# Performance work log

Hardware: AMD Instinct MI355X
Metric: run time of the kernel (lower is better)

The kernel has to match this reference:

```python
import jax, jax.numpy as jnp
import numpy as np
import math

B, S, D, H, L = 256, 256, 256, 4, 2
DH = D // H
NITEMS = 50000
EPS = 1e-5


def setup_inputs() -> dict:
    key = jax.random.key(0)
    ks = jax.random.split(key, 16)
    w = lambda k, shape, scale: (jax.random.normal(k, shape, jnp.float32) * scale)
    return {
        "input_ids": jax.random.randint(ks[0], (B, S), 0, NITEMS),
        "item_emb": w(ks[1], (NITEMS, D), 0.02),
        "pos_emb": w(ks[2], (S, D), 0.02),
        "Wq": w(ks[3], (L, D, D), 0.05),
        "bq": jnp.zeros((L, D), jnp.float32),
        "Wk": w(ks[4], (L, D, D), 0.05),
        "bk": jnp.zeros((L, D), jnp.float32),
        "Wv": w(ks[5], (L, D, D), 0.05),
        "bv": jnp.zeros((L, D), jnp.float32),
        "Wo": w(ks[6], (L, D, D), 0.05),
        "bo": jnp.zeros((L, D), jnp.float32),
        "W1": w(ks[7], (L, D, 4 * D), 0.05),
        "b1": jnp.zeros((L, 4 * D), jnp.float32),
        "W2": w(ks[8], (L, 4 * D, D), 0.05),
        "b2": jnp.zeros((L, D), jnp.float32),
    }


def _layer_norm(x):
    mu = jnp.mean(x, axis=-1, keepdims=True)
    var = jnp.mean(jnp.square(x - mu), axis=-1, keepdims=True)
    return (x - mu) * jax.lax.rsqrt(var + EPS)


def reference(input_ids, item_emb, pos_emb, Wq, bq, Wk, bk, Wv, bv,
              Wo, bo, W1, b1, W2, b2):
    Bn, Sn = input_ids.shape
    dtype = item_emb.dtype
    # attention bias: padding (id>0) AND causal; (1-mask)*-10000
    pad = (input_ids > 0).astype(dtype)                       # [B,S]
    causal = jnp.tril(jnp.ones((Sn, Sn), dtype))              # [S,S]
    mask = pad[:, None, None, :] * causal[None, None]         # [B,1,S,S]
    attn_bias = (1.0 - mask) * -10000.0

    # input embedding (dropout is identity in eval)
    x = _layer_norm(item_emb[input_ids] + pos_emb[None])      # [B,S,D]
    total = x
    scale = 1.0 / math.sqrt(DH)

    for l in range(L):
        # --- self-attention ---
        def heads(z):  # [B,S,D] -> [B,H,S,DH]
            return z.reshape(Bn, Sn, H, DH).transpose(0, 2, 1, 3)
        q = heads(x @ Wq[l] + bq[l])
        k = heads(x @ Wk[l] + bk[l])
        v = heads(x @ Wv[l] + bv[l])
        scores = jnp.einsum('bhqd,bhkd->bhqk', q, k) * scale + attn_bias
        probs = jax.nn.softmax(scores, axis=-1)
        ctx = jnp.einsum('bhqk,bhkd->bhqd', probs, v)
        ctx = ctx.transpose(0, 2, 1, 3).reshape(Bn, Sn, D)
        h = _layer_norm(ctx @ Wo[l] + bo[l] + x)
        # --- FFN (no residual in IntermediateLayer) ---
        ffn = jax.nn.gelu(h @ W1[l] + b1[l], approximate=False) @ W2[l] + b2[l]
        x = _layer_norm(ffn)
        total = total + x

    return total
```

## Files before the change

kernel.cpp:

```cpp
#include <hip/hip_runtime.h>
#include <math.h>

typedef __attribute__((ext_vector_type(8))) short short8;
typedef __attribute__((ext_vector_type(4))) short shortx4;
typedef __attribute__((ext_vector_type(4))) int   intx4;
typedef __attribute__((ext_vector_type(4))) float floatx4;

#define BQ 256
#define SQ 256
#define DQ 256
#define HQ 4
#define DHQ 64

__device__ __forceinline__ short f2bf(float f) {
  union { float f; unsigned u; } c; c.f = f;
  unsigned r = c.u + 0x7fffu + ((c.u >> 16) & 1u);
  return (short)(r >> 16);
}
__device__ __forceinline__ float bf2f(short s) {
  union { unsigned u; float f; } c; c.u = ((unsigned)(unsigned short)s) << 16;
  return c.f;
}
__device__ __forceinline__ float gelu_fast(float x) {
  float t = x * (0.7978845608f + 0.0356774081f * x * x);
  return x / (1.0f + __expf(-2.0f * t));
}

__device__ __forceinline__ void async16(const void* g, void* l) {
  __builtin_amdgcn_global_load_lds(
      (const __attribute__((address_space(1))) void*)g,
      (__attribute__((address_space(3))) void*)l, 16, 0, 0);
}

__global__ __launch_bounds__(256) void wconv_kernel(const float* __restrict__ W,
    short* __restrict__ Wt, int K, int N, int total) {
  int idx = blockIdx.x * 256 + threadIdx.x;
  if (idx >= total) return;
  int nk = N * K;
  int l = idx / nk;
  int r = idx - l * nk;
  int n = r / K;
  int k = r - n * K;
  Wt[idx] = f2bf(W[(size_t)l * nk + (size_t)k * N + n]);
}

__global__ __launch_bounds__(256) void wconv_qkv_kernel(const float* __restrict__ Wq,
    const float* __restrict__ Wk, const float* __restrict__ Wv, short* __restrict__ Wt) {
  int idx = blockIdx.x * 256 + threadIdx.x;
  int l = idx / 196608;
  int r = idx - l * 196608;
  int which = r / 65536;
  int e = r & 65535;
  int n = e >> 8, k = e & 255;
  const float* W = (which == 0) ? Wq : ((which == 1) ? Wk : Wv);
  Wt[idx] = f2bf(W[l * 65536 + k * 256 + n]);
}

__global__ __launch_bounds__(256) void bconv_kernel(const float* __restrict__ bq,
    const float* __restrict__ bk, const float* __restrict__ bv, float* __restrict__ dst) {
  int i = blockIdx.x * 256 + threadIdx.x;
  int l = i / 768, r = i - l * 768;
  const float* src = (r < 256) ? bq : ((r < 512) ? bk : bv);
  dst[i] = src[l * 256 + (r & 255)];
}

__global__ __launch_bounds__(256) void embed_kernel(const int* __restrict__ ids,
    const float* __restrict__ item, const float* __restrict__ pos,
    short* __restrict__ xb, float* __restrict__ tot) {
  const int tid = threadIdx.x, lane = tid & 63, w = tid >> 6;
  const int row = blockIdx.x * 4 + w;
  const int s = row & (SQ - 1);
  const int id = ids[row];
  floatx4 a = *(const floatx4*)(item + (size_t)id * DQ + lane * 4);
  floatx4 p = *(const floatx4*)(pos + (size_t)s * DQ + lane * 4);
  float v[4];
#pragma unroll
  for (int i = 0; i < 4; ++i) v[i] = a[i] + p[i];
  float sm = v[0] + v[1] + v[2] + v[3];
  float ss = v[0]*v[0] + v[1]*v[1] + v[2]*v[2] + v[3]*v[3];
#pragma unroll
  for (int off = 32; off; off >>= 1) { sm += __shfl_xor(sm, off); ss += __shfl_xor(ss, off); }
  float mu = sm * (1.0f / DQ);
  float var = ss * (1.0f / DQ) - mu * mu;
  float rs = rsqrtf(var + 1e-5f);
  shortx4 o; floatx4 y;
#pragma unroll
  for (int i = 0; i < 4; ++i) { y[i] = (v[i] - mu) * rs; o[i] = f2bf(y[i]); }
  *(shortx4*)(xb + (size_t)row * DQ + lane * 4) = o;
  *(floatx4*)(tot + (size_t)row * DQ + lane * 4) = y;
}

__global__ __launch_bounds__(512, 4) void gemm_kernel(
    const short* __restrict__ A, const short* __restrict__ Bt,
    const float* __restrict__ bias, const short* __restrict__ res,
    short* __restrict__ out, float* __restrict__ tot, short* __restrict__ vt,
    int M, int N, int K, int act, int ln, int chunked) {
  __shared__ short smem[12288];
  short* As = smem;
  short* Bs = smem + 4096;
  float* redS  = (float*)(smem + 8448);
  float* redS2 = redS + 512;
  const int tid = threadIdx.x, lane = tid & 63, w = tid >> 6;
  const int lane15 = lane & 15, quad = lane >> 4;
  const int wm = w & 1, wn = w >> 1;
  const int bm = blockIdx.y, bn = blockIdx.x;

  const int rA = lane >> 2;
  const int swzA = (rA & 3) ^ ((rA >> 2) & 3);
  const int gA = ((lane & 3) ^ swzA) * 8;
  const short* Ag  = A  + (size_t)(bm * 128 + w * 16 + rA) * K + gA;
  const short* Bg0 = Bt + (size_t)(bn * 256 + w * 32 + rA) * K + gA;
  const short* Bg1 = Bg0 + (size_t)16 * K;

  const int qs = ((quad ^ ((lane15 & 3) ^ ((lane15 >> 2) & 3))) * 8);

  floatx4 acc[4][4] = {};
  const int nk = K >> 5;
  for (int kb = 0; kb < nk; ++kb) {
    const int k0 = kb * 32;
    async16(Ag + k0, &As[w * 512]);
    async16(Bg0 + k0, &Bs[w * 1024]);
    async16(Bg1 + k0, &Bs[w * 1024 + 512]);
    __syncthreads();
    short8 af[4], bfr[4];
#pragma unroll
    for (int i = 0; i < 4; ++i) {
      af[i]  = *(const short8*)&As[(wm * 64 + i * 16 + lane15) * 32 + qs];
      bfr[i] = *(const short8*)&Bs[(wn * 64 + i * 16 + lane15) * 32 + qs];
    }
#pragma unroll
    for (int i = 0; i < 4; ++i)
#pragma unroll
      for (int j = 0; j < 4; ++j)
        acc[i][j] = __builtin_amdgcn_mfma_f32_16x16x32_bf16(bfr[j], af[i], acc[i][j], 0, 0, 0);
    __syncthreads();
  }

  float sum_[4], sq_[4];
#pragma unroll
  for (int i = 0; i < 4; ++i) { sum_[i] = 0.0f; sq_[i] = 0.0f; }
#pragma unroll
  for (int i = 0; i < 4; ++i) {
    size_t rowg = (size_t)bm * 128 + wm * 64 + i * 16 + lane15;
#pragma unroll
    for (int j = 0; j < 4; ++j) {
      int nloc = wn * 64 + j * 16 + quad * 4;
      floatx4 b4 = *(const floatx4*)(bias + bn * 256 + nloc);
      shortx4 r4;
      if (res) r4 = *(const shortx4*)(res + rowg * 256 + nloc);
#pragma unroll
      for (int r = 0; r < 4; ++r) {
        float z = acc[i][j][r] + b4[r];
        if (res) z += bf2f(r4[r]);
        if (act) z = gelu_fast(z);
        acc[i][j][r] = z;
        if (ln) { sum_[i] += z; sq_[i] += z * z; }
      }
    }
  }

  if (ln) {
#pragma unroll
    for (int i = 0; i < 4; ++i) {
      sum_[i] += __shfl_xor(sum_[i], 16); sum_[i] += __shfl_xor(sum_[i], 32);
      sq_[i]  += __shfl_xor(sq_[i], 16);  sq_[i]  += __shfl_xor(sq_[i], 32);
    }
    if (quad == 0) {
#pragma unroll
      for (int i = 0; i < 4; ++i) {
        int lr = wm * 64 + i * 16 + lane15;
        redS[lr * 4 + wn] = sum_[i];
        redS2[lr * 4 + wn] = sq_[i];
      }
    }
    __syncthreads();
#pragma unroll
    for (int i = 0; i < 4; ++i) {
      int lr = wm * 64 + i * 16 + lane15;
      float s = redS[lr * 4] + redS[lr * 4 + 1] + redS[lr * 4 + 2] + redS[lr * 4 + 3];
      float q = redS2[lr * 4] + redS2[lr * 4 + 1] + redS2[lr * 4 + 2] + redS2[lr * 4 + 3];
      float mu = s * (1.0f / 256.0f);
      float var = q * (1.0f / 256.0f) - mu * mu;
      float rs = rsqrtf(var + 1e-5f);
      size_t rowg = (size_t)bm * 128 + wm * 64 + i * 16 + lane15;
#pragma unroll
      for (int j = 0; j < 4; ++j) {
        int nloc = wn * 64 + j * 16 + quad * 4;
        floatx4 y;
#pragma unroll
        for (int r = 0; r < 4; ++r) y[r] = (acc[i][j][r] - mu) * rs;
        acc[i][j] = y;
        if (tot) {
          floatx4* tp = (floatx4*)(tot + rowg * 256 + nloc);
          floatx4 t = *tp;
#pragma unroll
          for (int r = 0; r < 4; ++r) t[r] += y[r];
          *tp = t;
        }
      }
    }
  }

  const int vtrans = (vt != nullptr) && (bn == 2);

#pragma unroll
  for (int i = 0; i < 4; ++i) {
    __syncthreads();
    int lr = wm * 16 + lane15;
#pragma unroll
    for (int j = 0; j < 4; ++j) {
      shortx4 o;
#pragma unroll
      for (int r = 0; r < 4; ++r) o[r] = f2bf(acc[i][j][r]);
      *(shortx4*)&smem[lr * 264 + wn * 64 + j * 16 + quad * 4] = o;
    }
    __syncthreads();
    if (vtrans) {
      int d = tid & 255;
      int grp = tid >> 8;
      short vv[16];
#pragma unroll
      for (int rr = 0; rr < 16; ++rr) vv[rr] = smem[(grp * 16 + rr) * 264 + d];
      size_t row = ((size_t)((bm >> 1) * 256 + d)) * 256 + (bm & 1) * 128 + grp * 64 + i * 16;
      *(short8*)(vt + row) = *(short8*)&vv[0];
      *(short8*)(vt + row + 8) = *(short8*)&vv[8];
    } else {
#pragma unroll
      for (int it = 0; it < 2; ++it) {
        int t2 = tid + it * 512;
        int lr2 = t2 >> 5, c = (t2 & 31) * 8;
        short8 v = *(const short8*)&smem[lr2 * 264 + c];
        size_t rowg = (size_t)bm * 128 + (lr2 >> 4) * 64 + i * 16 + (lr2 & 15);
        short* dst = chunked ? out + (size_t)bn * M * 256 + rowg * 256 + c
                             : out + rowg * (size_t)N + bn * 256 + c;
        *(short8*)dst = v;
      }
    }
  }
}

__global__ __launch_bounds__(256, 4) void attn_kernel(
    const short* __restrict__ qg, const short* __restrict__ kg,
    const short* __restrict__ vtg, const int* __restrict__ ids,
    short* __restrict__ ctxg) {
  __shared__ short lds[20480];
  const int tid = threadIdx.x, lane = tid & 63, w = tid >> 6;
  const int lane15 = lane & 15, quad = lane >> 4;
  const int l7 = lane15 & 7;
  const int bx = blockIdx.x;
  const int qh = bx & 1, h = (bx >> 1) & 3, b = bx >> 3;
  const int kbmax = qh * 2 + 1;

  short8 qf[2][2];
#pragma unroll
  for (int t = 0; t < 2; ++t) {
    int q0 = qh * 128 + t * 64 + w * 16;
#pragma unroll
    for (int ks = 0; ks < 2; ++ks)
      qf[t][ks] = *(const short8*)(qg + (size_t)(b * 256 + q0 + lane15) * 256 +
                                   h * 64 + ks * 32 + quad * 8);
  }

  float m_[2][4], l_[2][4];
  floatx4 o[2][4];
#pragma unroll
  for (int t = 0; t < 2; ++t)
#pragma unroll
    for (int r = 0; r < 4; ++r) {
      m_[t][r] = -1e30f; l_[t][r] = 0.0f;
#pragma unroll
      for (int dt = 0; dt < 4; ++dt) o[t][dt][r] = 0.0f;
    }

  const int srow = w * 8 + (lane >> 3);
  const int g8 = ((lane & 7) ^ (srow & 7)) * 8;
  const short* kgp = kg + (size_t)(b * 256 + srow) * 256 + h * 64 + g8;
  const short* vgp = vtg + (size_t)(b * 256 + h * 64 + srow) * 256 + g8;
  short* pbuf = &lds[16384 + w * 1024];

#define STAGE_TILE(kb_, ib_)                                                       \
  do {                                                                             \
    async16(kgp + (size_t)(kb_) * 64 * 256,        &lds[(ib_) * 4096 + w * 512]);  \
    async16(kgp + (size_t)((kb_) * 64 + 32) * 256, &lds[(ib_) * 4096 + 2048 + w * 512]); \
    async16(vgp + (kb_) * 64,            &lds[8192 + (ib_) * 4096 + w * 512]);     \
    async16(vgp + 32 * 256 + (kb_) * 64, &lds[8192 + (ib_) * 4096 + 2048 + w * 512]); \
  } while (0)

  STAGE_TILE(0, 0);

  for (int kb = 0; kb <= kbmax; ++kb) {
    __syncthreads();
    if (kb < kbmax) {
      int ib = (kb + 1) & 1;
      STAGE_TILE(kb + 1, ib);
    }
    const short* kbuf = &lds[(kb & 1) * 4096];
    const short* vbuf = &lds[8192 + (kb & 1) * 4096];

    float padb[4];
#pragma unroll
    for (int t16 = 0; t16 < 4; ++t16)
      padb[t16] = (ids[b * 256 + kb * 64 + t16 * 16 + lane15] > 0) ? 0.0f : -10000.0f;

#pragma unroll
    for (int t = 0; t < 2; ++t) {
      if (qh * 2 + t < kb) continue;
      const int q0 = qh * 128 + t * 64 + w * 16;
      const int diag = (qh * 2 + t == kb);
      floatx4 e[4];
#pragma unroll
      for (int t16 = 0; t16 < 4; ++t16) {
        floatx4 a = {0.f, 0.f, 0.f, 0.f};
#pragma unroll
        for (int ks = 0; ks < 2; ++ks) {
          short8 kf = *(const short8*)&kbuf[(t16 * 16 + lane15) * 64 +
                                            (((ks * 4 + quad) ^ l7) * 8)];
          a = __builtin_amdgcn_mfma_f32_16x16x32_bf16(qf[t][ks], kf, a, 0, 0, 0);
        }
        if (diag) {
          int kk = kb * 64 + t16 * 16 + lane15;
#pragma unroll
          for (int r = 0; r < 4; ++r) {
            int q = q0 + quad * 4 + r;
            e[t16][r] = a[r] * 0.125f + ((kk <= q) ? padb[t16] : -10000.0f);
          }
        } else {
#pragma unroll
          for (int r = 0; r < 4; ++r) e[t16][r] = a[r] * 0.125f + padb[t16];
        }
      }
#pragma unroll
      for (int r = 0; r < 4; ++r) {
        float mx = fmaxf(fmaxf(e[0][r], e[1][r]), fmaxf(e[2][r], e[3][r]));
        mx = fmaxf(mx, __shfl_xor(mx, 1));
        mx = fmaxf(mx, __shfl_xor(mx, 2));
        mx = fmaxf(mx, __shfl_xor(mx, 4));
        mx = fmaxf(mx, __shfl_xor(mx, 8));
        float mn = fmaxf(m_[t][r], mx);
        float alpha = __expf(m_[t][r] - mn);
        m_[t][r] = mn;
        float s = 0.0f;
#pragma unroll
        for (int t16 = 0; t16 < 4; ++t16) {
          float ev = __expf(e[t16][r] - mn);
          e[t16][r] = ev;
          s += ev;
        }
        s += __shfl_xor(s, 1); s += __shfl_xor(s, 2);
        s += __shfl_xor(s, 4); s += __shfl_xor(s, 8);
        l_[t][r] = l_[t][r] * alpha + s;
#pragma unroll
        for (int dt = 0; dt < 4; ++dt) o[t][dt][r] *= alpha;
        int qloc = quad * 4 + r;
        int swq = (qloc & 7) ^ (qloc >> 2);
#pragma unroll
        for (int t16 = 0; t16 < 4; ++t16) {
          int slot = (t16 * 2 + (lane15 >> 3)) ^ swq;
          pbuf[qloc * 64 + slot * 8 + l7] = f2bf(e[t16][r]);
        }
      }
#pragma unroll
      for (int kb2 = 0; kb2 < 2; ++kb2) {
        short8 pf = *(const short8*)&pbuf[lane15 * 64 +
                      ((((kb2 * 4 + quad) ^ l7 ^ (lane15 >> 2)) * 8))];
#pragma unroll
        for (int dt = 0; dt < 4; ++dt) {
          short8 vf = *(const short8*)&vbuf[(dt * 16 + lane15) * 64 +
                        (((kb2 * 4 + quad) ^ l7) * 8)];
          o[t][dt] = __builtin_amdgcn_mfma_f32_16x16x32_bf16(pf, vf, o[t][dt], 0, 0, 0);
        }
      }
    }
  }

#pragma unroll
  for (int t = 0; t < 2; ++t) {
    const int q0 = qh * 128 + t * 64 + w * 16;
#pragma unroll
    for (int r = 0; r < 4; ++r) {
      float inv = 1.0f / l_[t][r];
      size_t row = (size_t)(b * 256 + q0 + quad * 4 + r) * 256 + h * 64;
#pragma unroll
      for (int dt = 0; dt < 4; ++dt)
        ctxg[row + dt * 16 + lane15] = f2bf(o[t][dt][r] * inv);
    }
  }
}

extern "C" void kernel_launch(void* const* d_in, const int* in_sizes, int n_in,
                              void* d_out, int out_size, void* d_ws, size_t ws_size,
                              hipStream_t stream) {
  const int*   ids  = (const int*)d_in[0];
  const float* item = (const float*)d_in[1];
  const float* pos  = (const float*)d_in[2];
  const float* Wq = (const float*)d_in[3];  const float* bq = (const float*)d_in[4];
  const float* Wk = (const float*)d_in[5];  const float* bk = (const float*)d_in[6];
  const float* Wv = (const float*)d_in[7];  const float* bv = (const float*)d_in[8];
  const float* Wo = (const float*)d_in[9];  const float* bo = (const float*)d_in[10];
  const float* W1 = (const float*)d_in[11]; const float* b1 = (const float*)d_in[12];
  const float* W2 = (const float*)d_in[13]; const float* b2 = (const float*)d_in[14];
  float* out = (float*)d_out;

  const size_t EL = (size_t)BQ * SQ * DQ;
  short* qb    = (short*)d_ws;
  short* kb    = qb + EL;
  short* vt    = kb + EL;
  short* ctxb  = vt + EL;
  short* gb    = qb;
  short* xb    = ctxb + EL;
  short* hb    = xb + EL;
  short* WqkvT = hb + EL;
  short* WoT   = WqkvT + 2 * 3 * 65536;
  short* W1T   = WoT + 2 * 65536;
  short* W2T   = W1T + 2 * 262144;
  float* bqkv  = (float*)(W2T + 2 * 262144);

  const int M = BQ * SQ;

  wconv_qkv_kernel<<<1536, 256, 0, stream>>>(Wq, Wk, Wv, WqkvT);
  wconv_kernel<<<512, 256, 0, stream>>>(Wo, WoT, 256, 256, 131072);
  wconv_kernel<<<2048, 256, 0, stream>>>(W1, W1T, 256, 1024, 524288);
  wconv_kernel<<<2048, 256, 0, stream>>>(W2, W2T, 1024, 256, 524288);
  bconv_kernel<<<6, 256, 0, stream>>>(bq, bk, bv, bqkv);

  embed_kernel<<<M / 4, 256, 0, stream>>>(ids, item, pos, xb, out);

  for (int l = 0; l < 2; ++l) {
    gemm_kernel<<<dim3(3, M / 128), 512, 0, stream>>>(
        xb, WqkvT + (size_t)l * 3 * 65536, bqkv + l * 768, nullptr, qb, nullptr, vt,
        M, 768, 256, 0, 0, 1);
    attn_kernel<<<BQ * HQ * 2, 256, 0, stream>>>(qb, kb, vt, ids, ctxb);
    gemm_kernel<<<dim3(1, M / 128), 512, 0, stream>>>(
        ctxb, WoT + (size_t)l * 65536, bo + l * 256, xb, hb, nullptr, nullptr,
        M, 256, 256, 0, 1, 0);
    gemm_kernel<<<dim3(4, M / 128), 512, 0, stream>>>(
        hb, W1T + (size_t)l * 262144, b1 + l * 1024, nullptr, gb, nullptr, nullptr,
        M, 1024, 256, 1, 0, 0);
    gemm_kernel<<<dim3(1, M / 128), 512, 0, stream>>>(
        gb, W2T + (size_t)l * 262144, b2 + l * 256, nullptr, xb, out, nullptr,
        M, 256, 1024, 0, 1, 0);
  }
}
```

Before: 867.1 us.

## Rebalance causal attention, template GEMM epilogues, fuse weight transposes into one kernel

Attention now runs one 512-thread block per (batch, head), and each wave takes a paired short and long causal query strip (w and 15-w) so the triangular work is balanced. Fully masked key tiles on the diagonal are skipped, padding bias is staged once in LDS, and the context output is written through LDS as coalesced 16-byte stores. The GEMM flags become template parameters so dead epilogue branches compile away. The five weight and bias conversion kernels merge into one LDS-tiled transpose kernel. The larger attention blocks raise per-block LDS and register pressure and halve the block count.

Result: faster. 812.7 us (-6.3%).

```diff
diff --git a/kernel.cpp b/kernel.cpp
--- a/kernel.cpp
+++ b/kernel.cpp
@@ -3,14 +3,12 @@
 
 typedef __attribute__((ext_vector_type(8))) short short8;
 typedef __attribute__((ext_vector_type(4))) short shortx4;
-typedef __attribute__((ext_vector_type(4))) int   intx4;
 typedef __attribute__((ext_vector_type(4))) float floatx4;
 
 #define BQ 256
 #define SQ 256
 #define DQ 256
 #define HQ 4
-#define DHQ 64
 
 __device__ __forceinline__ short f2bf(float f) {
   union { float f; unsigned u; } c; c.f = f;
@@ -25,43 +23,59 @@
   float t = x * (0.7978845608f + 0.0356774081f * x * x);
   return x / (1.0f + __expf(-2.0f * t));
 }
-
 __device__ __forceinline__ void async16(const void* g, void* l) {
   __builtin_amdgcn_global_load_lds(
       (const __attribute__((address_space(1))) void*)g,
       (__attribute__((address_space(3))) void*)l, 16, 0, 0);
 }
 
-__global__ __launch_bounds__(256) void wconv_kernel(const float* __restrict__ W,
-    short* __restrict__ Wt, int K, int N, int total) {
-  int idx = blockIdx.x * 256 + threadIdx.x;
-  if (idx >= total) return;
-  int nk = N * K;
-  int l = idx / nk;
-  int r = idx - l * nk;
-  int n = r / K;
-  int k = r - n * K;
-  Wt[idx] = f2bf(W[(size_t)l * nk + (size_t)k * N + n]);
-}
-
-__global__ __launch_bounds__(256) void wconv_qkv_kernel(const float* __restrict__ Wq,
-    const float* __restrict__ Wk, const float* __restrict__ Wv, short* __restrict__ Wt) {
-  int idx = blockIdx.x * 256 + threadIdx.x;
-  int l = idx / 196608;
-  int r = idx - l * 196608;
-  int which = r / 65536;
-  int e = r & 65535;
-  int n = e >> 8, k = e & 255;
-  const float* W = (which == 0) ? Wq : ((which == 1) ? Wk : Wv);
-  Wt[idx] = f2bf(W[l * 65536 + k * 256 + n]);
-}
-
-__global__ __launch_bounds__(256) void bconv_kernel(const float* __restrict__ bq,
-    const float* __restrict__ bk, const float* __restrict__ bv, float* __restrict__ dst) {
-  int i = blockIdx.x * 256 + threadIdx.x;
-  int l = i / 768, r = i - l * 768;
-  const float* src = (r < 256) ? bq : ((r < 512) ? bk : bv);
-  dst[i] = src[l * 256 + (r & 255)];
+__global__ __launch_bounds__(256) void wtrans_kernel(
+    const float* __restrict__ Wq, const float* __restrict__ Wk, const float* __restrict__ Wv,
+    const float* __restrict__ Wo, const float* __restrict__ W1, const float* __restrict__ W2,
+    const float* __restrict__ bq, const float* __restrict__ bk, const float* __restrict__ bv,
+    short* __restrict__ WqkvT, short* __restrict__ WoT, short* __restrict__ W1T,
+    short* __restrict__ W2T, float* __restrict__ bqkv) {
+  const int bid = blockIdx.x, tid = threadIdx.x;
+  if (bid >= 384) {
+    int i = bid - 384;
+    int l = i / 3, which = i - l * 3;
+    const float* src = (which == 0) ? bq : ((which == 1) ? bk : bv);
+    bqkv[l * 768 + which * 256 + tid] = src[l * 256 + tid];
+    return;
+  }
+  __shared__ float t[64][65];
+  const float* src; short* dst; int K, N, tile;
+  if (bid < 96)       { int l = bid / 48, r = bid % 48, which = r / 16; tile = r % 16;
+    src = ((which == 0) ? Wq : (which == 1) ? Wk : Wv) + l * 65536;
+    dst = WqkvT + (l * 3 + which) * 65536; K = 256; N = 256; }
+  else if (bid < 128) { int i = bid - 96, l = i / 16; tile = i % 16;
+    src = Wo + l * 65536; dst = WoT + l * 65536; K = 256; N = 256; }
+  else if (bid < 256) { int i = bid - 128, l = i / 64; tile = i % 64;
+    src = W1 + l * 262144; dst = W1T + l * 262144; K = 256; N = 1024; }
+  else                { int i = bid - 256, l = i / 64; tile = i % 64;
+    src = W2 + l * 262144; dst = W2T + l * 262144; K = 1024; N = 256; }
+  const int ntj = N >> 6;
+  const int ti = tile / ntj, tj = tile - ti * ntj;
+  {
+    int r = tid >> 2, c0 = (tid & 3) * 16;
+    const float* sp = src + (size_t)(ti * 64 + r) * N + tj * 64 + c0;
+#pragma unroll
+    for (int j = 0; j < 4; ++j) {
+      floatx4 v = *(const floatx4*)(sp + j * 4);
+      t[r][c0 + j * 4 + 0] = v[0]; t[r][c0 + j * 4 + 1] = v[1];
+      t[r][c0 + j * 4 + 2] = v[2]; t[r][c0 + j * 4 + 3] = v[3];
+    }
+  }
+  __syncthreads();
+  {
+    int d = tid & 63, ch = tid >> 6;
+    short8 o[2];
+#pragma unroll
+    for (int j = 0; j < 16; ++j) o[j >> 3][j & 7] = f2bf(t[ch * 16 + j][d]);
+    short* dp = dst + (size_t)(tj * 64 + d) * K + ti * 64 + ch * 16;
+    *(short8*)dp = o[0];
+    *(short8*)(dp + 8) = o[1];
+  }
 }
 
 __global__ __launch_bounds__(256) void embed_kernel(const int* __restrict__ ids,
@@ -90,11 +104,12 @@
   *(floatx4*)(tot + (size_t)row * DQ + lane * 4) = y;
 }
 
+template <int ACT, int LN, int RES, int TOT, int SMODE>
 __global__ __launch_bounds__(512, 4) void gemm_kernel(
     const short* __restrict__ A, const short* __restrict__ Bt,
     const float* __restrict__ bias, const short* __restrict__ res,
     short* __restrict__ out, float* __restrict__ tot, short* __restrict__ vt,
-    int M, int N, int K, int act, int ln, int chunked) {
+    int M, int N, int K) {
   __shared__ short smem[12288];
   short* As = smem;
   short* Bs = smem + 4096;
@@ -111,7 +126,6 @@
   const short* Ag  = A  + (size_t)(bm * 128 + w * 16 + rA) * K + gA;
   const short* Bg0 = Bt + (size_t)(bn * 256 + w * 32 + rA) * K + gA;
   const short* Bg1 = Bg0 + (size_t)16 * K;
-
   const int qs = ((quad ^ ((lane15 & 3) ^ ((lane15 >> 2) & 3))) * 8);
 
   floatx4 acc[4][4] = {};
@@ -147,19 +161,19 @@
       int nloc = wn * 64 + j * 16 + quad * 4;
       floatx4 b4 = *(const floatx4*)(bias + bn * 256 + nloc);
       shortx4 r4;
-      if (res) r4 = *(const shortx4*)(res + rowg * 256 + nloc);
+      if (RES) r4 = *(const shortx4*)(res + rowg * 256 + nloc);
 #pragma unroll
       for (int r = 0; r < 4; ++r) {
         float z = acc[i][j][r] + b4[r];
-        if (res) z += bf2f(r4[r]);
-        if (act) z = gelu_fast(z);
+        if (RES) z += bf2f(r4[r]);
+        if (ACT) z = gelu_fast(z);
         acc[i][j][r] = z;
-        if (ln) { sum_[i] += z; sq_[i] += z * z; }
-      }
-    }
-  }
-
-  if (ln) {
+        if (LN) { sum_[i] += z; sq_[i] += z * z; }
+      }
+    }
+  }
+
+  if (LN) {
 #pragma unroll
     for (int i = 0; i < 4; ++i) {
       sum_[i] += __shfl_xor(sum_[i], 16); sum_[i] += __shfl_xor(sum_[i], 32);
@@ -190,7 +204,7 @@
 #pragma unroll
         for (int r = 0; r < 4; ++r) y[r] = (acc[i][j][r] - mu) * rs;
         acc[i][j] = y;
-        if (tot) {
+        if (TOT) {
           floatx4* tp = (floatx4*)(tot + rowg * 256 + nloc);
           floatx4 t = *tp;
 #pragma unroll
@@ -201,8 +215,6 @@
     }
   }
 
-  const int vtrans = (vt != nullptr) && (bn == 2);
-
 #pragma unroll
   for (int i = 0; i < 4; ++i) {
     __syncthreads();
@@ -215,7 +227,7 @@
       *(shortx4*)&smem[lr * 264 + wn * 64 + j * 16 + quad * 4] = o;
     }
     __syncthreads();
-    if (vtrans) {
+    if (SMODE == 1 && bn == 2) {
       int d = tid & 255;
       int grp = tid >> 8;
       short vv[16];
@@ -231,126 +243,119 @@
         int lr2 = t2 >> 5, c = (t2 & 31) * 8;
         short8 v = *(const short8*)&smem[lr2 * 264 + c];
         size_t rowg = (size_t)bm * 128 + (lr2 >> 4) * 64 + i * 16 + (lr2 & 15);
-        short* dst = chunked ? out + (size_t)bn * M * 256 + rowg * 256 + c
-                             : out + rowg * (size_t)N + bn * 256 + c;
+        short* dst = (SMODE == 1) ? out + (size_t)bn * M * 256 + rowg * 256 + c
+                                  : out + rowg * (size_t)N + bn * 256 + c;
         *(short8*)dst = v;
       }
     }
   }
 }
 
-__global__ __launch_bounds__(256, 4) void attn_kernel(
+__global__ __launch_bounds__(512, 4) void attn_kernel(
     const short* __restrict__ qg, const short* __restrict__ kg,
     const short* __restrict__ vtg, const int* __restrict__ ids,
     short* __restrict__ ctxg) {
-  __shared__ short lds[20480];
+  __shared__ short lds[25088];
+  float* padS = (float*)&lds[24576];
   const int tid = threadIdx.x, lane = tid & 63, w = tid >> 6;
-  const int lane15 = lane & 15, quad = lane >> 4;
-  const int l7 = lane15 & 7;
-  const int bx = blockIdx.x;
-  const int qh = bx & 1, h = (bx >> 1) & 3, b = bx >> 3;
-  const int kbmax = qh * 2 + 1;
-
+  const int lane15 = lane & 15, quad = lane >> 4, l7 = lane15 & 7;
+  const int h = blockIdx.x & 3, b = blockIdx.x >> 2;
+
+  if (tid < 256) padS[tid] = (ids[b * 256 + tid] > 0) ? 0.0f : -10000.0f;
+
+  const int stA[2] = {w, 15 - w};
   short8 qf[2][2];
 #pragma unroll
-  for (int t = 0; t < 2; ++t) {
-    int q0 = qh * 128 + t * 64 + w * 16;
+  for (int tt = 0; tt < 2; ++tt) {
+    int q0 = stA[tt] * 16;
 #pragma unroll
     for (int ks = 0; ks < 2; ++ks)
-      qf[t][ks] = *(const short8*)(qg + (size_t)(b * 256 + q0 + lane15) * 256 +
-                                   h * 64 + ks * 32 + quad * 8);
+      qf[tt][ks] = *(const short8*)(qg + (size_t)(b * 256 + q0 + lane15) * 256 +
+                                    h * 64 + ks * 32 + quad * 8);
   }
 
   float m_[2][4], l_[2][4];
   floatx4 o[2][4];
 #pragma unroll
-  for (int t = 0; t < 2; ++t)
+  for (int tt = 0; tt < 2; ++tt)
 #pragma unroll
     for (int r = 0; r < 4; ++r) {
-      m_[t][r] = -1e30f; l_[t][r] = 0.0f;
-#pragma unroll
-      for (int dt = 0; dt < 4; ++dt) o[t][dt][r] = 0.0f;
-    }
-
-  const int srow = w * 8 + (lane >> 3);
-  const int g8 = ((lane & 7) ^ (srow & 7)) * 8;
+      m_[tt][r] = -1e30f; l_[tt][r] = 0.0f;
+#pragma unroll
+      for (int dt = 0; dt < 4; ++dt) o[tt][dt][r] = 0.0f;
+    }
+
+  const int srow = tid >> 3;
+  const int g8 = ((tid & 7) ^ (srow & 7)) * 8;
   const short* kgp = kg + (size_t)(b * 256 + srow) * 256 + h * 64 + g8;
   const short* vgp = vtg + (size_t)(b * 256 + h * 64 + srow) * 256 + g8;
   short* pbuf = &lds[16384 + w * 1024];
 
-#define STAGE_TILE(kb_, ib_)                                                       \
-  do {                                                                             \
-    async16(kgp + (size_t)(kb_) * 64 * 256,        &lds[(ib_) * 4096 + w * 512]);  \
-    async16(kgp + (size_t)((kb_) * 64 + 32) * 256, &lds[(ib_) * 4096 + 2048 + w * 512]); \
-    async16(vgp + (kb_) * 64,            &lds[8192 + (ib_) * 4096 + w * 512]);     \
-    async16(vgp + 32 * 256 + (kb_) * 64, &lds[8192 + (ib_) * 4096 + 2048 + w * 512]); \
+#define STG(kb_, ib_)                                                     \
+  do {                                                                    \
+    async16(kgp + (size_t)(kb_) * 64 * 256, &lds[(ib_) * 4096 + w * 512]);\
+    async16(vgp + (kb_) * 64, &lds[8192 + (ib_) * 4096 + w * 512]);       \
   } while (0)
 
-  STAGE_TILE(0, 0);
-
-  for (int kb = 0; kb <= kbmax; ++kb) {
-    __syncthreads();
-    if (kb < kbmax) {
-      int ib = (kb + 1) & 1;
-      STAGE_TILE(kb + 1, ib);
-    }
+  STG(0, 0);
+
+  for (int kb = 0; kb < 4; ++kb) {
+    __syncthreads();
+    if (kb < 3) STG(kb + 1, (kb + 1) & 1);
     const short* kbuf = &lds[(kb & 1) * 4096];
     const short* vbuf = &lds[8192 + (kb & 1) * 4096];
 
-    float padb[4];
-#pragma unroll
-    for (int t16 = 0; t16 < 4; ++t16)
-      padb[t16] = (ids[b * 256 + kb * 64 + t16 * 16 + lane15] > 0) ? 0.0f : -10000.0f;
-
-#pragma unroll
-    for (int t = 0; t < 2; ++t) {
-      if (qh * 2 + t < kb) continue;
-      const int q0 = qh * 128 + t * 64 + w * 16;
-      const int diag = (qh * 2 + t == kb);
+#pragma unroll
+    for (int tt = 0; tt < 2; ++tt) {
+      const int st = stA[tt];
+      if (st < 4 * kb) continue;
+      const int q0 = st * 16;
+      const int diag = (st >> 2) == kb;
+      const int stlo = st & 3;
       floatx4 e[4];
 #pragma unroll
       for (int t16 = 0; t16 < 4; ++t16) {
+        if (diag && t16 > stlo) {
+          e[t16] = (floatx4){-1e30f, -1e30f, -1e30f, -1e30f};
+          continue;
+        }
         floatx4 a = {0.f, 0.f, 0.f, 0.f};
 #pragma unroll
         for (int ks = 0; ks < 2; ++ks) {
           short8 kf = *(const short8*)&kbuf[(t16 * 16 + lane15) * 64 +
                                             (((ks * 4 + quad) ^ l7) * 8)];
-          a = __builtin_amdgcn_mfma_f32_16x16x32_bf16(qf[t][ks], kf, a, 0, 0, 0);
-        }
-        if (diag) {
+          a = __builtin_amdgcn_mfma_f32_16x16x32_bf16(qf[tt][ks], kf, a, 0, 0, 0);
+        }
+        float pb = padS[kb * 64 + t16 * 16 + lane15];
+        if (diag && t16 == stlo) {
           int kk = kb * 64 + t16 * 16 + lane15;
 #pragma unroll
-          for (int r = 0; r < 4; ++r) {
-            int q = q0 + quad * 4 + r;
-            e[t16][r] = a[r] * 0.125f + ((kk <= q) ? padb[t16] : -10000.0f);
-          }
+          for (int r = 0; r < 4; ++r)
+            e[t16][r] = a[r] * 0.125f + ((kk <= q0 + quad * 4 + r) ? pb : -10000.0f);
         } else {
 #pragma unroll
-          for (int r = 0; r < 4; ++r) e[t16][r] = a[r] * 0.125f + padb[t16];
+          for (int r = 0; r < 4; ++r) e[t16][r] = a[r] * 0.125f + pb;
         }
       }
 #pragma unroll
       for (int r = 0; r < 4; ++r) {
         float mx = fmaxf(fmaxf(e[0][r], e[1][r]), fmaxf(e[2][r], e[3][r]));
-        mx = fmaxf(mx, __shfl_xor(mx, 1));
-        mx = fmaxf(mx, __shfl_xor(mx, 2));
-        mx = fmaxf(mx, __shfl_xor(mx, 4));
-        mx = fmaxf(mx, __shfl_xor(mx, 8));
-        float mn = fmaxf(m_[t][r], mx);
-        float alpha = __expf(m_[t][r] - mn);
-        m_[t][r] = mn;
+        mx = fmaxf(mx, __shfl_xor(mx, 1)); mx = fmaxf(mx, __shfl_xor(mx, 2));
+        mx = fmaxf(mx, __shfl_xor(mx, 4)); mx = fmaxf(mx, __shfl_xor(mx, 8));
+        float mn = fmaxf(m_[tt][r], mx);
+        float alpha = __expf(m_[tt][r] - mn);
+        m_[tt][r] = mn;
         float s = 0.0f;
 #pragma unroll
         for (int t16 = 0; t16 < 4; ++t16) {
           float ev = __expf(e[t16][r] - mn);
-          e[t16][r] = ev;
-          s += ev;
+          e[t16][r] = ev; s += ev;
         }
         s += __shfl_xor(s, 1); s += __shfl_xor(s, 2);
         s += __shfl_xor(s, 4); s += __shfl_xor(s, 8);
-        l_[t][r] = l_[t][r] * alpha + s;
-#pragma unroll
-        for (int dt = 0; dt < 4; ++dt) o[t][dt][r] *= alpha;
+        l_[tt][r] = l_[tt][r] * alpha + s;
+#pragma unroll
+        for (int dt = 0; dt < 4; ++dt) o[tt][dt][r] *= alpha;
         int qloc = quad * 4 + r;
         int swq = (qloc & 7) ^ (qloc >> 2);
 #pragma unroll
@@ -362,27 +367,35 @@
 #pragma unroll
       for (int kb2 = 0; kb2 < 2; ++kb2) {
         short8 pf = *(const short8*)&pbuf[lane15 * 64 +
-                      ((((kb2 * 4 + quad) ^ l7 ^ (lane15 >> 2)) * 8))];
+                      (((kb2 * 4 + quad) ^ l7 ^ (lane15 >> 2)) * 8)];
 #pragma unroll
         for (int dt = 0; dt < 4; ++dt) {
           short8 vf = *(const short8*)&vbuf[(dt * 16 + lane15) * 64 +
                         (((kb2 * 4 + quad) ^ l7) * 8)];
-          o[t][dt] = __builtin_amdgcn_mfma_f32_16x16x32_bf16(pf, vf, o[t][dt], 0, 0, 0);
-        }
-      }
-    }
-  }
-
-#pragma unroll
-  for (int t = 0; t < 2; ++t) {
-    const int q0 = qh * 128 + t * 64 + w * 16;
+          o[tt][dt] = __builtin_amdgcn_mfma_f32_16x16x32_bf16(pf, vf, o[tt][dt], 0, 0, 0);
+        }
+      }
+    }
+  }
+
+#pragma unroll
+  for (int tt = 0; tt < 2; ++tt) {
+    const int q0 = stA[tt] * 16;
 #pragma unroll
     for (int r = 0; r < 4; ++r) {
-      float inv = 1.0f / l_[t][r];
-      size_t row = (size_t)(b * 256 + q0 + quad * 4 + r) * 256 + h * 64;
+      int qloc = quad * 4 + r;
+      float inv = 1.0f / l_[tt][r];
 #pragma unroll
       for (int dt = 0; dt < 4; ++dt)
-        ctxg[row + dt * 16 + lane15] = f2bf(o[t][dt][r] * inv);
+        pbuf[qloc * 64 + ((dt ^ quad) * 16) + lane15] = f2bf(o[tt][dt][r] * inv);
+    }
+#pragma unroll
+    for (int it = 0; it < 2; ++it) {
+      int idx = it * 64 + lane;
+      int row = idx >> 3, u = idx & 7;
+      int d0 = (((u >> 1) ^ (row >> 2)) << 4) + (u & 1) * 8;
+      short8 v = *(const short8*)&pbuf[row * 64 + u * 8];
+      *(short8*)(ctxg + (size_t)(b * 256 + q0 + row) * 256 + h * 64 + d0) = v;
     }
   }
 }
@@ -403,8 +416,8 @@
 
   const size_t EL = (size_t)BQ * SQ * DQ;
   short* qb    = (short*)d_ws;
-  short* kb    = qb + EL;
-  short* vt    = kb + EL;
+  short* kb_   = qb + EL;
+  short* vt    = kb_ + EL;
   short* ctxb  = vt + EL;
   short* gb    = qb;
   short* xb    = ctxb + EL;
@@ -417,27 +430,23 @@
 
   const int M = BQ * SQ;
 
-  wconv_qkv_kernel<<<1536, 256, 0, stream>>>(Wq, Wk, Wv, WqkvT);
-  wconv_kernel<<<512, 256, 0, stream>>>(Wo, WoT, 256, 256, 131072);
-  wconv_kernel<<<2048, 256, 0, stream>>>(W1, W1T, 256, 1024, 524288);
-  wconv_kernel<<<2048, 256, 0, stream>>>(W2, W2T, 1024, 256, 524288);
-  bconv_kernel<<<6, 256, 0, stream>>>(bq, bk, bv, bqkv);
-
+  wtrans_kernel<<<390, 256, 0, stream>>>(Wq, Wk, Wv, Wo, W1, W2, bq, bk, bv,
+                                         WqkvT, WoT, W1T, W2T, bqkv);
   embed_kernel<<<M / 4, 256, 0, stream>>>(ids, item, pos, xb, out);
 
   for (int l = 0; l < 2; ++l) {
-    gemm_kernel<<<dim3(3, M / 128), 512, 0, stream>>>(
+    gemm_kernel<0, 0, 0, 0, 1><<<dim3(3, M / 128), 512, 0, stream>>>(
         xb, WqkvT + (size_t)l * 3 * 65536, bqkv + l * 768, nullptr, qb, nullptr, vt,
-        M, 768, 256, 0, 0, 1);
-    attn_kernel<<<BQ * HQ * 2, 256, 0, stream>>>(qb, kb, vt, ids, ctxb);
-    gemm_kernel<<<dim3(1, M / 128), 512, 0, stream>>>(
+        M, 768, 256);
+    attn_kernel<<<BQ * HQ, 512, 0, stream>>>(qb, kb_, vt, ids, ctxb);
+    gemm_kernel<0, 1, 1, 0, 0><<<dim3(1, M / 128), 512, 0, stream>>>(
         ctxb, WoT + (size_t)l * 65536, bo + l * 256, xb, hb, nullptr, nullptr,
-        M, 256, 256, 0, 1, 0);
-    gemm_kernel<<<dim3(4, M / 128), 512, 0, stream>>>(
+        M, 256, 256);
+    gemm_kernel<1, 0, 0, 0, 0><<<dim3(4, M / 128), 512, 0, stream>>>(
         hb, W1T + (size_t)l * 262144, b1 + l * 1024, nullptr, gb, nullptr, nullptr,
-        M, 1024, 256, 1, 0, 0);
-    gemm_kernel<<<dim3(1, M / 128), 512, 0, stream>>>(
+        M, 1024, 256);
+    gemm_kernel<0, 1, 0, 1, 0><<<dim3(1, M / 128), 512, 0, stream>>>(
         gb, W2T + (size_t)l * 262144, b2 + l * 256, nullptr, xb, out, nullptr,
-        M, 256, 1024, 0, 1, 0);
-  }
-}
+        M, 256, 1024);
+  }
+}
```
